# Kernel optimization log

Measured on AMD Instinct MI355X. Metric: run time of the kernel, lower is better.

## Reference

```python
import jax, jax.numpy as jnp
import numpy as np

B, T, D = 2, 1024, 2048
E, K, H = 64, 4, 512          # n_experts, top-k, expert_dim
S, HS = 2, H * K              # shared experts, shared hidden dim
CAP = 512


def setup_inputs() -> dict:
    key = jax.random.key(0)
    ks = jax.random.split(key, 9)
    scale = 0.02
    return {
        "x": jax.random.normal(ks[0], (B, T, D), jnp.float32),
        "Wr": jax.random.normal(ks[1], (D, E), jnp.float32) * scale,
        "router_bias": jnp.zeros((E,), jnp.float32),
        "Wg": jax.random.normal(ks[2], (E, D, H), jnp.float32) * scale,
        "Wu": jax.random.normal(ks[3], (E, D, H), jnp.float32) * scale,
        "Wd": jax.random.normal(ks[4], (E, H, D), jnp.float32) * scale,
        "Sg": jax.random.normal(ks[5], (S, D, HS), jnp.float32) * scale,
        "Su": jax.random.normal(ks[6], (S, D, HS), jnp.float32) * scale,
        "Sd": jax.random.normal(ks[7], (S, HS, D), jnp.float32) * scale,
    }


def reference(x, Wr, router_bias, Wg, Wu, Wd, Sg, Su, Sd):
    Bx, Tx, Dx = x.shape
    N = Bx * Tx
    flat = x.reshape(N, Dx)                              # [N, D]

    # ---- router ----
    logits = flat @ Wr + router_bias                     # [N, E]
    scores = jax.nn.softmax(logits, axis=-1)
    topk_scores, topk_idx = jax.lax.top_k(scores, K)     # [N, K]
    topk_scores = topk_scores / topk_scores.sum(-1, keepdims=True)

    eid = topk_idx.reshape(-1)                           # [N*K] expert per assignment
    w = topk_scores.reshape(-1)                          # [N*K] combine weight
    tok = jnp.repeat(jnp.arange(N), K)                   # [N*K] source token id

    # position of each assignment within its expert's buffer
    oh = jax.nn.one_hot(eid, E, dtype=jnp.int32)         # [N*K, E]
    pos = ((jnp.cumsum(oh, axis=0) * oh).sum(-1) - 1)    # [N*K]
    valid = pos < CAP

    # ---- dispatch: scatter tokens into per-expert buffers ----
    xb = jnp.zeros((E, CAP, Dx), x.dtype).at[eid, pos].set(flat[tok], mode="drop")

    # ---- grouped SwiGLU expert FFN ----
    h = jax.nn.silu(jnp.einsum("ecd,edh->ech", xb, Wg)) * jnp.einsum("ecd,edh->ech", xb, Wu)
    yb = jnp.einsum("ech,ehd->ecd", h, Wd)               # [E, CAP, D]

    # ---- combine: gather back and weighted scatter-add to tokens ----
    y = yb[eid, jnp.minimum(pos, CAP - 1)] * (w * valid)[:, None]
    out = jnp.zeros((N, Dx), x.dtype).at[tok].add(y)

    # ---- always-on shared experts ----
    hs = jax.nn.silu(jnp.einsum("nd,sdh->nsh", flat, Sg)) * jnp.einsum("nd,sdh->nsh", flat, Su)
    out = out + jnp.einsum("nsh,shd->nd", hs, Sd)

    return out.reshape(Bx, Tx, Dx)
```

## Files before the change

### kernel.cpp

```cpp
#include <hip/hip_runtime.h>
#include <hip/hip_bf16.h>
#include <stdint.h>

#define N_TOK 2048
#define DM    2048
#define NEXP  64
#define TOPK  4
#define HEXP  512
#define CAPC  512
#define NSH   2
#define HSH   2048
#define RTB   8

typedef __attribute__((ext_vector_type(8))) short short8;
typedef __attribute__((ext_vector_type(4))) float f32x4;
typedef __attribute__((ext_vector_type(4))) float f4;

#define GLDS16(g, l) __builtin_amdgcn_global_load_lds(                     \
    (const __attribute__((address_space(1))) void*)(g),                    \
    (__attribute__((address_space(3))) void*)(l), 16, 0, 0)

static __device__ __forceinline__ unsigned short f2bf(float f) {
  union { float f; unsigned u; } v; v.f = f;
  unsigned r = v.u + 0x7FFFu + ((v.u >> 16) & 1u);
  return (unsigned short)(r >> 16);
}

__global__ __launch_bounds__(256) void k_convert(const float* __restrict__ x,
                                                 unsigned short* __restrict__ xb) {
  int i = (blockIdx.x * 256 + threadIdx.x) * 8;
  f4 a = *(const f4*)(x + i);
  f4 b = *(const f4*)(x + i + 4);
  short8 o;
  o[0]=f2bf(a[0]); o[1]=f2bf(a[1]); o[2]=f2bf(a[2]); o[3]=f2bf(a[3]);
  o[4]=f2bf(b[0]); o[5]=f2bf(b[1]); o[6]=f2bf(b[2]); o[7]=f2bf(b[3]);
  *(short8*)(xb + i) = o;
}

#define ARGMAX_ROUND(S,I)                                            \
  { float bv = v; int bi = lane;                                     \
    _Pragma("unroll")                                                \
    for (int o = 32; o; o >>= 1) {                                   \
      float ov = __shfl_xor(bv, o); int oi = __shfl_xor(bi, o);      \
      if (ov > bv || (ov == bv && oi < bi)) { bv = ov; bi = oi; }    \
    }                                                                \
    S = bv; I = bi; if (lane == bi) v = -1.f; }

__global__ __launch_bounds__(256) void k_router(const float* __restrict__ x,
    const float* __restrict__ Wr, const float* __restrict__ bias,
    int* __restrict__ cnt, int* __restrict__ lists, float* __restrict__ wlist) {
  __shared__ float part[4][RTB][64];
  __shared__ float logits[RTB][64];
  int t = threadIdx.x;
  int e = t & 63, sl = t >> 6;
  int tok0 = blockIdx.x * RTB;
  const float* xp = x + (size_t)tok0 * DM;
  float acc[RTB];
#pragma unroll
  for (int i = 0; i < RTB; ++i) acc[i] = 0.f;
  for (int d = sl * 512; d < sl * 512 + 512; ++d) {
    float w = Wr[(size_t)d * NEXP + e];
#pragma unroll
    for (int i = 0; i < RTB; ++i) acc[i] += xp[(size_t)i * DM + d] * w;
  }
#pragma unroll
  for (int i = 0; i < RTB; ++i) part[sl][i][e] = acc[i];
  __syncthreads();
  for (int i = sl; i < RTB; i += 4)
    logits[i][e] = part[0][i][e] + part[1][i][e] + part[2][i][e] + part[3][i][e] + bias[e];
  __syncthreads();
  int lane = t & 63, wv = t >> 6;
  for (int i = wv * 2; i < wv * 2 + 2; ++i) {
    float lg = logits[i][lane];
    float m = lg;
#pragma unroll
    for (int o = 32; o; o >>= 1) m = fmaxf(m, __shfl_xor(m, o));
    float p = expf(lg - m);
    float sm = p;
#pragma unroll
    for (int o = 32; o; o >>= 1) sm += __shfl_xor(sm, o);
    float v = p / sm;
    float s0, s1, s2, s3; int i0, i1, i2, i3;
    ARGMAX_ROUND(s0, i0)
    ARGMAX_ROUND(s1, i1)
    ARGMAX_ROUND(s2, i2)
    ARGMAX_ROUND(s3, i3)
    float tot = s0 + s1 + s2 + s3;
    if (lane < TOPK) {
      float myw = (lane == 0 ? s0 : lane == 1 ? s1 : lane == 2 ? s2 : s3) / tot;
      int   mye = (lane == 0 ? i0 : lane == 1 ? i1 : lane == 2 ? i2 : i3);
      int pos = atomicAdd(&cnt[mye], 1);
      if (pos < CAPC) {
        lists[mye * CAPC + pos] = tok0 + i;
        wlist[mye * CAPC + pos] = myw;
      }
    }
  }
}

__global__ void k_offs(const int* __restrict__ cnt, int* __restrict__ offs) {
  int l = threadIdx.x;
  int c = min(cnt[l], CAPC);
  int sum = c;
#pragma unroll
  for (int o = 1; o < 64; o <<= 1) {
    int ov = __shfl_up(sum, o);
    if (l >= o) sum += ov;
  }
  offs[l + 1] = sum;
  if (l == 0) offs[0] = 0;
}


static __device__ __forceinline__ short8 frag_ldA(const unsigned short* lds, int row, int kElem) {
  int byte = row * 128 + kElem * 2;
  byte ^= (row & 7) << 4;
  return *(const short8*)((const char*)lds + byte);
}

static __device__ __forceinline__ short8 bfragB(const float* lB, int nl, int kb) {
  short8 r;
#pragma unroll
  for (int j = 0; j < 8; ++j) r[j] = (short)f2bf(lB[(kb + j) * 64 + nl]);
  return r;
}

static __device__ __forceinline__ void mma1f(const unsigned short* lA, const float* lB,
    f32x4 (&acc)[4][2], int wm, int wn, int lane) {
  int r16 = lane & 15;
  int kg  = (lane >> 4) * 8;
#pragma unroll
  for (int kk = 0; kk < 2; ++kk) {
    int kb = kk * 32 + kg;
    short8 a[4], b[2];
#pragma unroll
    for (int mf = 0; mf < 4; ++mf) a[mf] = frag_ldA(lA, wm + mf * 16 + r16, kb);
#pragma unroll
    for (int nf = 0; nf < 2; ++nf) b[nf] = bfragB(lB, wn + nf * 16 + r16, kb);
#pragma unroll
    for (int mf = 0; mf < 4; ++mf)
#pragma unroll
      for (int nf = 0; nf < 2; ++nf)
        acc[mf][nf] = __builtin_amdgcn_mfma_f32_16x16x32_bf16(a[mf], b[nf], acc[mf][nf], 0, 0, 0);
  }
}

static __device__ __forceinline__ void mma2f(const unsigned short* lA,
    const float* lBg, const float* lBu,
    f32x4 (&accg)[4][2], f32x4 (&accu)[4][2], int wm, int wn, int lane) {
  int r16 = lane & 15;
  int kg  = (lane >> 4) * 8;
#pragma unroll
  for (int kk = 0; kk < 2; ++kk) {
    int kb = kk * 32 + kg;
    short8 a[4], bg[2], bu[2];
#pragma unroll
    for (int mf = 0; mf < 4; ++mf) a[mf] = frag_ldA(lA, wm + mf * 16 + r16, kb);
#pragma unroll
    for (int nf = 0; nf < 2; ++nf) {
      bg[nf] = bfragB(lBg, wn + nf * 16 + r16, kb);
      bu[nf] = bfragB(lBu, wn + nf * 16 + r16, kb);
    }
#pragma unroll
    for (int mf = 0; mf < 4; ++mf)
#pragma unroll
      for (int nf = 0; nf < 2; ++nf) {
        accg[mf][nf] = __builtin_amdgcn_mfma_f32_16x16x32_bf16(a[mf], bg[nf], accg[mf][nf], 0, 0, 0);
        accu[mf][nf] = __builtin_amdgcn_mfma_f32_16x16x32_bf16(a[mf], bu[nf], accu[mf][nf], 0, 0, 0);
      }
  }
}

static __device__ __forceinline__ float silu_mul(float g, float u) {
  return g / (1.f + expf(-g)) * u;
}

#define A_SETUP(asrc, SROW_EXPR)                                            \
  const unsigned short* asrc[4];                                            \
  {                                                                         \
    _Pragma("unroll")                                                       \
    for (int p = 0; p < 4; ++p) {                                           \
      int row = wv * 32 + p * 8 + (lane >> 3);                              \
      int srow = (SROW_EXPR);                                               \
      asrc[p] = Abase + (size_t)srow * lda + (((lane & 7) ^ (row & 7)) << 3);\
    }                                                                       \
  }

#define B_SETUP(bsrc, Bbase, ldb)                                           \
  const float* bsrc[4];                                                     \
  {                                                                         \
    _Pragma("unroll")                                                       \
    for (int p = 0; p < 4; ++p) {                                           \
      int k = wv * 16 + p * 4 + (lane >> 4);                                \
      bsrc[p] = (Bbase) + (size_t)k * (ldb) + n0 + (lane & 15) * 4;         \
    }                                                                       \
  }

#define A_STAGE(asrc, lA, k0)                                               \
  _Pragma("unroll")                                                         \
  for (int p = 0; p < 4; ++p) GLDS16(asrc[p] + (k0), (lA) + wv * 2048 + p * 512);

#define B_STAGE(bsrc, lB, k0, ldb)                                          \
  _Pragma("unroll")                                                         \
  for (int p = 0; p < 4; ++p) GLDS16(bsrc[p] + (size_t)(k0) * (ldb), (lB) + wv * 1024 + p * 256);

__global__ __launch_bounds__(256, 3) void k_expert_gateup(const unsigned short* __restrict__ xbf,
    const float* __restrict__ Wg, const float* __restrict__ Wu,
    const int* __restrict__ cnt, const int* __restrict__ offs,
    const int* __restrict__ lists, unsigned short* __restrict__ hws) {
  int e = blockIdx.y;
  int ne = min(cnt[e], CAPC);
  if (ne == 0) return;
  int n0 = blockIdx.x * 64;
  const float* Bg = Wg + (size_t)e * DM * HEXP;
  const float* Bu = Wu + (size_t)e * DM * HEXP;
  const int* lst = lists + e * CAPC;
  int base = offs[e];
  __shared__ unsigned short lA[128 * 64];
  __shared__ float lBg[64 * 64];
  __shared__ float lBu[64 * 64];
  int tid = threadIdx.x;
  int lane = tid & 63, wv = tid >> 6;
  int wm = (wv >> 1) * 64, wn = (wv & 1) * 32;
  const unsigned short* Abase = xbf; const int lda = DM;
  B_SETUP(bgsrc, Bg, HEXP)
  B_SETUP(busrc, Bu, HEXP)
  for (int m0 = 0; m0 < ne; m0 += 128) {
    A_SETUP(asrc, lst[min(m0 + row, ne - 1)])
    f32x4 accg[4][2] = {};
    f32x4 accu[4][2] = {};
    for (int k0 = 0; k0 < DM; k0 += 64) {
      A_STAGE(asrc, lA, k0)
      B_STAGE(bgsrc, lBg, k0, HEXP)
      B_STAGE(busrc, lBu, k0, HEXP)
      __syncthreads();
      mma2f(lA, lBg, lBu, accg, accu, wm, wn, lane);
      __syncthreads();
    }
#pragma unroll
    for (int mf = 0; mf < 4; ++mf)
#pragma unroll
      for (int r = 0; r < 4; ++r) {
        int rl = m0 + wm + mf * 16 + (lane >> 4) * 4 + r;
        if (rl < ne) {
#pragma unroll
          for (int nf = 0; nf < 2; ++nf) {
            int col = n0 + wn + nf * 16 + (lane & 15);
            float h = silu_mul(accg[mf][nf][r], accu[mf][nf][r]);
            hws[(size_t)(base + rl) * HEXP + col] = f2bf(h);
          }
        }
      }
  }
}

__global__ __launch_bounds__(256, 3) void k_shared_gateup(const unsigned short* __restrict__ xbf,
    const float* __restrict__ Sg, const float* __restrict__ Su,
    unsigned short* __restrict__ hs) {
  int n0 = blockIdx.x * 64;
  int m0 = blockIdx.y * 128;
  int s  = blockIdx.z;
  const float* Bg = Sg + (size_t)s * DM * HSH;
  const float* Bu = Su + (size_t)s * DM * HSH;
  __shared__ unsigned short lA[128 * 64];
  __shared__ float lBg[64 * 64];
  __shared__ float lBu[64 * 64];
  int tid = threadIdx.x;
  int lane = tid & 63, wv = tid >> 6;
  int wm = (wv >> 1) * 64, wn = (wv & 1) * 32;
  const unsigned short* Abase = xbf; const int lda = DM;
  B_SETUP(bgsrc, Bg, HSH)
  B_SETUP(busrc, Bu, HSH)
  A_SETUP(asrc, m0 + row)
  f32x4 accg[4][2] = {};
  f32x4 accu[4][2] = {};
  for (int k0 = 0; k0 < DM; k0 += 64) {
    A_STAGE(asrc, lA, k0)
    B_STAGE(bgsrc, lBg, k0, HSH)
    B_STAGE(busrc, lBu, k0, HSH)
    __syncthreads();
    mma2f(lA, lBg, lBu, accg, accu, wm, wn, lane);
    __syncthreads();
  }
#pragma unroll
  for (int mf = 0; mf < 4; ++mf)
#pragma unroll
    for (int nf = 0; nf < 2; ++nf)
#pragma unroll
      for (int r = 0; r < 4; ++r) {
        int row = m0 + wm + mf * 16 + (lane >> 4) * 4 + r;
        int col = n0 + wn + nf * 16 + (lane & 15);
        float h = silu_mul(accg[mf][nf][r], accu[mf][nf][r]);
        hs[(size_t)row * (NSH * HSH) + s * HSH + col] = f2bf(h);
      }
}

__global__ __launch_bounds__(256, 3) void k_shared_down(const unsigned short* __restrict__ hs,
    const float* __restrict__ Sd, float* __restrict__ out) {
  int n0 = blockIdx.x * 64;
  int m0 = blockIdx.y * 128;
  __shared__ unsigned short lA[128 * 64];
  __shared__ float lB[64 * 64];
  int tid = threadIdx.x;
  int lane = tid & 63, wv = tid >> 6;
  int wm = (wv >> 1) * 64, wn = (wv & 1) * 32;
  const unsigned short* Abase = hs; const int lda = NSH * HSH;
  B_SETUP(bsrc, Sd, DM)
  A_SETUP(asrc, m0 + row)
  f32x4 acc[4][2] = {};
  for (int k0 = 0; k0 < NSH * HSH; k0 += 64) {
    A_STAGE(asrc, lA, k0)
    B_STAGE(bsrc, lB, k0, DM)
    __syncthreads();
    mma1f(lA, lB, acc, wm, wn, lane);
    __syncthreads();
  }
#pragma unroll
  for (int mf = 0; mf < 4; ++mf)
#pragma unroll
    for (int nf = 0; nf < 2; ++nf)
#pragma unroll
      for (int r = 0; r < 4; ++r) {
        int row = m0 + wm + mf * 16 + (lane >> 4) * 4 + r;
        int col = n0 + wn + nf * 16 + (lane & 15);
        out[(size_t)row * DM + col] = acc[mf][nf][r];
      }
}

__global__ __launch_bounds__(256, 3) void k_expert_down(const unsigned short* __restrict__ hws,
    const float* __restrict__ Wd, const int* __restrict__ cnt, const int* __restrict__ offs,
    const int* __restrict__ lists, const float* __restrict__ wlist,
    float* __restrict__ out) {
  int e = blockIdx.y;
  int ne = min(cnt[e], CAPC);
  if (ne == 0) return;
  int n0 = blockIdx.x * 64;
  const float* B = Wd + (size_t)e * HEXP * DM;
  __shared__ unsigned short lA[128 * 64];
  __shared__ float lB[64 * 64];
  int tid = threadIdx.x;
  int lane = tid & 63, wv = tid >> 6;
  int wm = (wv >> 1) * 64, wn = (wv & 1) * 32;
  const unsigned short* Abase = hws + (size_t)offs[e] * HEXP; const int lda = HEXP;
  B_SETUP(bsrc, B, DM)
  for (int m0 = 0; m0 < ne; m0 += 128) {
    A_SETUP(asrc, min(m0 + row, ne - 1))
    f32x4 acc[4][2] = {};
    for (int k0 = 0; k0 < HEXP; k0 += 64) {
      A_STAGE(asrc, lA, k0)
      B_STAGE(bsrc, lB, k0, DM)
      __syncthreads();
      mma1f(lA, lB, acc, wm, wn, lane);
      __syncthreads();
    }
#pragma unroll
    for (int mf = 0; mf < 4; ++mf)
#pragma unroll
      for (int r = 0; r < 4; ++r) {
        int rl = m0 + wm + mf * 16 + (lane >> 4) * 4 + r;
        if (rl < ne) {
          int tok  = lists[e * CAPC + rl];
          float w  = wlist[e * CAPC + rl];
#pragma unroll
          for (int nf = 0; nf < 2; ++nf) {
            int col = n0 + wn + nf * 16 + (lane & 15);
            atomicAdd(out + (size_t)tok * DM + col, acc[mf][nf][r] * w);
          }
        }
      }
  }
}

extern "C" void kernel_launch(void* const* d_in, const int* in_sizes, int n_in,
                              void* d_out, int out_size, void* d_ws, size_t ws_size,
                              hipStream_t stream) {
  const float* x    = (const float*)d_in[0];
  const float* Wr   = (const float*)d_in[1];
  const float* bias = (const float*)d_in[2];
  const float* Wg   = (const float*)d_in[3];
  const float* Wu   = (const float*)d_in[4];
  const float* Wd   = (const float*)d_in[5];
  const float* Sg   = (const float*)d_in[6];
  const float* Su   = (const float*)d_in[7];
  const float* Sd   = (const float*)d_in[8];
  float* out = (float*)d_out;
  char* ws = (char*)d_ws;

  const size_t off_cnt   = 0;
  const size_t off_offs  = 256;
  const size_t off_lists = 1024;
  const size_t off_wlist = off_lists + (size_t)NEXP * CAPC * 4;
  const size_t off_xbf   = off_wlist + (size_t)NEXP * CAPC * 4;
  const size_t off_hs    = off_xbf + (size_t)N_TOK * DM * 2;
  const size_t off_h     = off_hs + (size_t)N_TOK * NSH * HSH * 2;
  const size_t req       = off_h + (size_t)N_TOK * TOPK * HEXP * 2;
  if (ws_size < req) return;

  int* cnt            = (int*)(ws + off_cnt);
  int* offs           = (int*)(ws + off_offs);
  int* lists          = (int*)(ws + off_lists);
  float* wlist        = (float*)(ws + off_wlist);
  unsigned short* xbf = (unsigned short*)(ws + off_xbf);
  unsigned short* hs  = (unsigned short*)(ws + off_hs);
  unsigned short* hws = (unsigned short*)(ws + off_h);

  hipMemsetAsync(cnt, 0, NEXP * sizeof(int), stream);
  k_convert<<<(N_TOK * DM) / (256 * 8), 256, 0, stream>>>(x, xbf);
  k_router<<<N_TOK / RTB, 256, 0, stream>>>(x, Wr, bias, cnt, lists, wlist);
  k_offs<<<1, 64, 0, stream>>>(cnt, offs);
  k_expert_gateup<<<dim3(HEXP / 64, NEXP), 256, 0, stream>>>(xbf, Wg, Wu, cnt, offs, lists, hws);
  k_shared_gateup<<<dim3(HSH / 64, N_TOK / 128, NSH), 256, 0, stream>>>(xbf, Sg, Su, hs);
  k_shared_down<<<dim3(DM / 64, N_TOK / 128), 256, 0, stream>>>(hs, Sd, out);
  k_expert_down<<<dim3(DM / 64, NEXP), 256, 0, stream>>>(hws, Wd, cnt, offs, lists, wlist, out);
}
```

Baseline: 670.9 us.

## Double-buffer LDS staging with BK=32 and swizzled B layout in GEMM kernels

Splits the K-tile from 64 to 32 and double-buffers A/B tiles in LDS so global-to-LDS loads for the next tile overlap MFMA work on the current one, with explicit vmcnt waits and raw barriers in place of __syncthreads. The A and B LDS layouts get new XOR swizzles meant to cut bank conflicts, and B fragment conversion switches to packed v_cvt_pk_bf16_f32. Down-projection kernels raise their occupancy hint to 4 blocks. In exchange there are more barriers per K step and hand-written waitcnt logic, which could race if the counts are wrong.

```diff
diff --git a/kernel.cpp b/kernel.cpp
--- a/kernel.cpp
+++ b/kernel.cpp
@@ -15,10 +15,16 @@
 typedef __attribute__((ext_vector_type(8))) short short8;
 typedef __attribute__((ext_vector_type(4))) float f32x4;
 typedef __attribute__((ext_vector_type(4))) float f4;
+typedef __attribute__((ext_vector_type(4))) unsigned uint4v;
 
 #define GLDS16(g, l) __builtin_amdgcn_global_load_lds(                     \
     (const __attribute__((address_space(1))) void*)(g),                    \
     (__attribute__((address_space(3))) void*)(l), 16, 0, 0)
+
+#define VMWAIT(N) asm volatile("s_waitcnt vmcnt(" #N ")" ::: "memory")
+#define BARX() do { asm volatile("" ::: "memory");                          \
+                    __builtin_amdgcn_s_barrier();                           \
+                    asm volatile("" ::: "memory"); } while (0)
 
 static __device__ __forceinline__ unsigned short f2bf(float f) {
   union { float f; unsigned u; } v; v.f = f;
@@ -113,62 +119,60 @@
 
 
 static __device__ __forceinline__ short8 frag_ldA(const unsigned short* lds, int row, int kElem) {
-  int byte = row * 128 + kElem * 2;
-  byte ^= (row & 7) << 4;
+  int byte = row * 64 + kElem * 2;
+  byte ^= ((row >> 1) & 3) << 4;
   return *(const short8*)((const char*)lds + byte);
 }
 
 static __device__ __forceinline__ short8 bfragB(const float* lB, int nl, int kb) {
-  short8 r;
-#pragma unroll
-  for (int j = 0; j < 8; ++j) r[j] = (short)f2bf(lB[(kb + j) * 64 + nl]);
-  return r;
+  const float* p = lB + kb * 64 + (nl ^ (((kb >> 3) & 1) << 4));
+  float f0 = p[0],   f1 = p[64],  f2 = p[128], f3 = p[192];
+  float f4_ = p[256], f5 = p[320], f6 = p[384], f7 = p[448];
+  unsigned u0, u1, u2, u3;
+  asm("v_cvt_pk_bf16_f32 %0, %1, %2" : "=v"(u0) : "v"(f0),  "v"(f1));
+  asm("v_cvt_pk_bf16_f32 %0, %1, %2" : "=v"(u1) : "v"(f2),  "v"(f3));
+  asm("v_cvt_pk_bf16_f32 %0, %1, %2" : "=v"(u2) : "v"(f4_), "v"(f5));
+  asm("v_cvt_pk_bf16_f32 %0, %1, %2" : "=v"(u3) : "v"(f6),  "v"(f7));
+  uint4v uv = {u0, u1, u2, u3};
+  return __builtin_bit_cast(short8, uv);
 }
 
 static __device__ __forceinline__ void mma1f(const unsigned short* lA, const float* lB,
     f32x4 (&acc)[4][2], int wm, int wn, int lane) {
   int r16 = lane & 15;
-  int kg  = (lane >> 4) * 8;
-#pragma unroll
-  for (int kk = 0; kk < 2; ++kk) {
-    int kb = kk * 32 + kg;
-    short8 a[4], b[2];
-#pragma unroll
-    for (int mf = 0; mf < 4; ++mf) a[mf] = frag_ldA(lA, wm + mf * 16 + r16, kb);
-#pragma unroll
-    for (int nf = 0; nf < 2; ++nf) b[nf] = bfragB(lB, wn + nf * 16 + r16, kb);
-#pragma unroll
-    for (int mf = 0; mf < 4; ++mf)
-#pragma unroll
-      for (int nf = 0; nf < 2; ++nf)
-        acc[mf][nf] = __builtin_amdgcn_mfma_f32_16x16x32_bf16(a[mf], b[nf], acc[mf][nf], 0, 0, 0);
-  }
+  int kb  = (lane >> 4) * 8;
+  short8 a[4], b[2];
+#pragma unroll
+  for (int mf = 0; mf < 4; ++mf) a[mf] = frag_ldA(lA, wm + mf * 16 + r16, kb);
+#pragma unroll
+  for (int nf = 0; nf < 2; ++nf) b[nf] = bfragB(lB, wn + nf * 16 + r16, kb);
+#pragma unroll
+  for (int mf = 0; mf < 4; ++mf)
+#pragma unroll
+    for (int nf = 0; nf < 2; ++nf)
+      acc[mf][nf] = __builtin_amdgcn_mfma_f32_16x16x32_bf16(a[mf], b[nf], acc[mf][nf], 0, 0, 0);
 }
 
 static __device__ __forceinline__ void mma2f(const unsigned short* lA,
     const float* lBg, const float* lBu,
     f32x4 (&accg)[4][2], f32x4 (&accu)[4][2], int wm, int wn, int lane) {
   int r16 = lane & 15;
-  int kg  = (lane >> 4) * 8;
-#pragma unroll
-  for (int kk = 0; kk < 2; ++kk) {
-    int kb = kk * 32 + kg;
-    short8 a[4], bg[2], bu[2];
-#pragma unroll
-    for (int mf = 0; mf < 4; ++mf) a[mf] = frag_ldA(lA, wm + mf * 16 + r16, kb);
+  int kb  = (lane >> 4) * 8;
+  short8 a[4], bg[2], bu[2];
+#pragma unroll
+  for (int mf = 0; mf < 4; ++mf) a[mf] = frag_ldA(lA, wm + mf * 16 + r16, kb);
+#pragma unroll
+  for (int nf = 0; nf < 2; ++nf) {
+    bg[nf] = bfragB(lBg, wn + nf * 16 + r16, kb);
+    bu[nf] = bfragB(lBu, wn + nf * 16 + r16, kb);
+  }
+#pragma unroll
+  for (int mf = 0; mf < 4; ++mf)
 #pragma unroll
     for (int nf = 0; nf < 2; ++nf) {
-      bg[nf] = bfragB(lBg, wn + nf * 16 + r16, kb);
-      bu[nf] = bfragB(lBu, wn + nf * 16 + r16, kb);
-    }
-#pragma unroll
-    for (int mf = 0; mf < 4; ++mf)
-#pragma unroll
-      for (int nf = 0; nf < 2; ++nf) {
-        accg[mf][nf] = __builtin_amdgcn_mfma_f32_16x16x32_bf16(a[mf], bg[nf], accg[mf][nf], 0, 0, 0);
-        accu[mf][nf] = __builtin_amdgcn_mfma_f32_16x16x32_bf16(a[mf], bu[nf], accu[mf][nf], 0, 0, 0);
-      }
-  }
+      accg[mf][nf] = __builtin_amdgcn_mfma_f32_16x16x32_bf16(a[mf], bg[nf], accg[mf][nf], 0, 0, 0);
+      accu[mf][nf] = __builtin_amdgcn_mfma_f32_16x16x32_bf16(a[mf], bu[nf], accu[mf][nf], 0, 0, 0);
+    }
 }
 
 static __device__ __forceinline__ float silu_mul(float g, float u) {
@@ -176,33 +180,35 @@
 }
 
 #define A_SETUP(asrc, SROW_EXPR)                                            \
-  const unsigned short* asrc[4];                                            \
+  const unsigned short* asrc[2];                                            \
   {                                                                         \
     _Pragma("unroll")                                                       \
-    for (int p = 0; p < 4; ++p) {                                           \
-      int row = wv * 32 + p * 8 + (lane >> 3);                              \
+    for (int p = 0; p < 2; ++p) {                                           \
+      int row = p * 64 + wv * 16 + (lane >> 2);                             \
       int srow = (SROW_EXPR);                                               \
-      asrc[p] = Abase + (size_t)srow * lda + (((lane & 7) ^ (row & 7)) << 3);\
+      asrc[p] = Abase + (size_t)srow * lda                                  \
+              + (((lane & 3) ^ ((row >> 1) & 3)) << 3);                     \
     }                                                                       \
   }
+#define A_STAGE(asrc, lAbuf, k0)                                            \
+  { _Pragma("unroll")                                                       \
+    for (int p = 0; p < 2; ++p)                                             \
+      GLDS16(asrc[p] + (k0), (lAbuf) + p * 2048 + wv * 512); }
 
 #define B_SETUP(bsrc, Bbase, ldb)                                           \
-  const float* bsrc[4];                                                     \
+  const float* bsrc[2];                                                     \
   {                                                                         \
     _Pragma("unroll")                                                       \
-    for (int p = 0; p < 4; ++p) {                                           \
-      int k = wv * 16 + p * 4 + (lane >> 4);                                \
-      bsrc[p] = (Bbase) + (size_t)k * (ldb) + n0 + (lane & 15) * 4;         \
+    for (int p = 0; p < 2; ++p) {                                           \
+      int k = p * 16 + wv * 4 + (lane >> 4);                                \
+      int c = (lane & 15) ^ (((k >> 3) & 1) << 2);                          \
+      bsrc[p] = (Bbase) + (size_t)k * (ldb) + n0 + c * 4;                   \
     }                                                                       \
   }
-
-#define A_STAGE(asrc, lA, k0)                                               \
-  _Pragma("unroll")                                                         \
-  for (int p = 0; p < 4; ++p) GLDS16(asrc[p] + (k0), (lA) + wv * 2048 + p * 512);
-
-#define B_STAGE(bsrc, lB, k0, ldb)                                          \
-  _Pragma("unroll")                                                         \
-  for (int p = 0; p < 4; ++p) GLDS16(bsrc[p] + (size_t)(k0) * (ldb), (lB) + wv * 1024 + p * 256);
+#define B_STAGE(bsrc, lBbuf, k0, ldb)                                       \
+  { _Pragma("unroll")                                                       \
+    for (int p = 0; p < 2; ++p)                                             \
+      GLDS16(bsrc[p] + (size_t)(k0) * (ldb), (lBbuf) + p * 1024 + wv * 256); }
 
 __global__ __launch_bounds__(256, 3) void k_expert_gateup(const unsigned short* __restrict__ xbf,
     const float* __restrict__ Wg, const float* __restrict__ Wu,
@@ -216,27 +222,45 @@
   const float* Bu = Wu + (size_t)e * DM * HEXP;
   const int* lst = lists + e * CAPC;
   int base = offs[e];
-  __shared__ unsigned short lA[128 * 64];
-  __shared__ float lBg[64 * 64];
-  __shared__ float lBu[64 * 64];
+  __shared__ unsigned short lA[2][128 * 32];
+  __shared__ float lBg[2][32 * 64];
+  __shared__ float lBu[2][32 * 64];
   int tid = threadIdx.x;
   int lane = tid & 63, wv = tid >> 6;
   int wm = (wv >> 1) * 64, wn = (wv & 1) * 32;
   const unsigned short* Abase = xbf; const int lda = DM;
   B_SETUP(bgsrc, Bg, HEXP)
   B_SETUP(busrc, Bu, HEXP)
+  const int NT = DM / 32;
   for (int m0 = 0; m0 < ne; m0 += 128) {
     A_SETUP(asrc, lst[min(m0 + row, ne - 1)])
     f32x4 accg[4][2] = {};
     f32x4 accu[4][2] = {};
-    for (int k0 = 0; k0 < DM; k0 += 64) {
-      A_STAGE(asrc, lA, k0)
-      B_STAGE(bgsrc, lBg, k0, HEXP)
-      B_STAGE(busrc, lBu, k0, HEXP)
-      __syncthreads();
-      mma2f(lA, lBg, lBu, accg, accu, wm, wn, lane);
-      __syncthreads();
-    }
+    A_STAGE(asrc, lA[0], 0)  B_STAGE(bgsrc, lBg[0], 0, HEXP)  B_STAGE(busrc, lBu[0], 0, HEXP)
+    A_STAGE(asrc, lA[1], 32) B_STAGE(bgsrc, lBg[1], 32, HEXP) B_STAGE(busrc, lBu[1], 32, HEXP)
+    VMWAIT(6); BARX();
+#pragma unroll 1
+    for (int t = 0; t < NT; t += 2) {
+      mma2f(lA[0], lBg[0], lBu[0], accg, accu, wm, wn, lane);
+      BARX();
+      if (t + 2 < NT) {
+        int k2 = (t + 2) * 32;
+        A_STAGE(asrc, lA[0], k2) B_STAGE(bgsrc, lBg[0], k2, HEXP) B_STAGE(busrc, lBu[0], k2, HEXP)
+        VMWAIT(6);
+      } else { VMWAIT(0); }
+      BARX();
+      mma2f(lA[1], lBg[1], lBu[1], accg, accu, wm, wn, lane);
+      if (t + 2 < NT) {
+        BARX();
+        if (t + 3 < NT) {
+          int k3 = (t + 3) * 32;
+          A_STAGE(asrc, lA[1], k3) B_STAGE(bgsrc, lBg[1], k3, HEXP) B_STAGE(busrc, lBu[1], k3, HEXP)
+          VMWAIT(6);
+        } else { VMWAIT(0); }
+        BARX();
+      }
+    }
+    BARX();
 #pragma unroll
     for (int mf = 0; mf < 4; ++mf)
 #pragma unroll
@@ -262,9 +286,9 @@
   int s  = blockIdx.z;
   const float* Bg = Sg + (size_t)s * DM * HSH;
   const float* Bu = Su + (size_t)s * DM * HSH;
-  __shared__ unsigned short lA[128 * 64];
-  __shared__ float lBg[64 * 64];
-  __shared__ float lBu[64 * 64];
+  __shared__ unsigned short lA[2][128 * 32];
+  __shared__ float lBg[2][32 * 64];
+  __shared__ float lBu[2][32 * 64];
   int tid = threadIdx.x;
   int lane = tid & 63, wv = tid >> 6;
   int wm = (wv >> 1) * 64, wn = (wv & 1) * 32;
@@ -274,13 +298,30 @@
   A_SETUP(asrc, m0 + row)
   f32x4 accg[4][2] = {};
   f32x4 accu[4][2] = {};
-  for (int k0 = 0; k0 < DM; k0 += 64) {
-    A_STAGE(asrc, lA, k0)
-    B_STAGE(bgsrc, lBg, k0, HSH)
-    B_STAGE(busrc, lBu, k0, HSH)
-    __syncthreads();
-    mma2f(lA, lBg, lBu, accg, accu, wm, wn, lane);
-    __syncthreads();
+  const int NT = DM / 32;
+  A_STAGE(asrc, lA[0], 0)  B_STAGE(bgsrc, lBg[0], 0, HSH)  B_STAGE(busrc, lBu[0], 0, HSH)
+  A_STAGE(asrc, lA[1], 32) B_STAGE(bgsrc, lBg[1], 32, HSH) B_STAGE(busrc, lBu[1], 32, HSH)
+  VMWAIT(6); BARX();
+#pragma unroll 1
+  for (int t = 0; t < NT; t += 2) {
+    mma2f(lA[0], lBg[0], lBu[0], accg, accu, wm, wn, lane);
+    BARX();
+    if (t + 2 < NT) {
+      int k2 = (t + 2) * 32;
+      A_STAGE(asrc, lA[0], k2) B_STAGE(bgsrc, lBg[0], k2, HSH) B_STAGE(busrc, lBu[0], k2, HSH)
+      VMWAIT(6);
+    } else { VMWAIT(0); }
+    BARX();
+    mma2f(lA[1], lBg[1], lBu[1], accg, accu, wm, wn, lane);
+    if (t + 2 < NT) {
+      BARX();
+      if (t + 3 < NT) {
+        int k3 = (t + 3) * 32;
+        A_STAGE(asrc, lA[1], k3) B_STAGE(bgsrc, lBg[1], k3, HSH) B_STAGE(busrc, lBu[1], k3, HSH)
+        VMWAIT(6);
+      } else { VMWAIT(0); }
+      BARX();
+    }
   }
 #pragma unroll
   for (int mf = 0; mf < 4; ++mf)
@@ -295,12 +336,12 @@
       }
 }
 
-__global__ __launch_bounds__(256, 3) void k_shared_down(const unsigned short* __restrict__ hs,
+__global__ __launch_bounds__(256, 4) void k_shared_down(const unsigned short* __restrict__ hs,
     const float* __restrict__ Sd, float* __restrict__ out) {
   int n0 = blockIdx.x * 64;
   int m0 = blockIdx.y * 128;
-  __shared__ unsigned short lA[128 * 64];
-  __shared__ float lB[64 * 64];
+  __shared__ unsigned short lA[2][128 * 32];
+  __shared__ float lB[2][32 * 64];
   int tid = threadIdx.x;
   int lane = tid & 63, wv = tid >> 6;
   int wm = (wv >> 1) * 64, wn = (wv & 1) * 32;
@@ -308,12 +349,30 @@
   B_SETUP(bsrc, Sd, DM)
   A_SETUP(asrc, m0 + row)
   f32x4 acc[4][2] = {};
-  for (int k0 = 0; k0 < NSH * HSH; k0 += 64) {
-    A_STAGE(asrc, lA, k0)
-    B_STAGE(bsrc, lB, k0, DM)
-    __syncthreads();
-    mma1f(lA, lB, acc, wm, wn, lane);
-    __syncthreads();
+  const int NT = (NSH * HSH) / 32;
+  A_STAGE(asrc, lA[0], 0)  B_STAGE(bsrc, lB[0], 0, DM)
+  A_STAGE(asrc, lA[1], 32) B_STAGE(bsrc, lB[1], 32, DM)
+  VMWAIT(4); BARX();
+#pragma unroll 1
+  for (int t = 0; t < NT; t += 2) {
+    mma1f(lA[0], lB[0], acc, wm, wn, lane);
+    BARX();
+    if (t + 2 < NT) {
+      int k2 = (t + 2) * 32;
+      A_STAGE(asrc, lA[0], k2) B_STAGE(bsrc, lB[0], k2, DM)
+      VMWAIT(4);
+    } else { VMWAIT(0); }
+    BARX();
+    mma1f(lA[1], lB[1], acc, wm, wn, lane);
+    if (t + 2 < NT) {
+      BARX();
+      if (t + 3 < NT) {
+        int k3 = (t + 3) * 32;
+        A_STAGE(asrc, lA[1], k3) B_STAGE(bsrc, lB[1], k3, DM)
+        VMWAIT(4);
+      } else { VMWAIT(0); }
+      BARX();
+    }
   }
 #pragma unroll
   for (int mf = 0; mf < 4; ++mf)
@@ -327,7 +386,7 @@
       }
 }
 
-__global__ __launch_bounds__(256, 3) void k_expert_down(const unsigned short* __restrict__ hws,
+__global__ __launch_bounds__(256, 4) void k_expert_down(const unsigned short* __restrict__ hws,
     const float* __restrict__ Wd, const int* __restrict__ cnt, const int* __restrict__ offs,
     const int* __restrict__ lists, const float* __restrict__ wlist,
     float* __restrict__ out) {
@@ -336,23 +395,42 @@
   if (ne == 0) return;
   int n0 = blockIdx.x * 64;
   const float* B = Wd + (size_t)e * HEXP * DM;
-  __shared__ unsigned short lA[128 * 64];
-  __shared__ float lB[64 * 64];
+  __shared__ unsigned short lA[2][128 * 32];
+  __shared__ float lB[2][32 * 64];
   int tid = threadIdx.x;
   int lane = tid & 63, wv = tid >> 6;
   int wm = (wv >> 1) * 64, wn = (wv & 1) * 32;
   const unsigned short* Abase = hws + (size_t)offs[e] * HEXP; const int lda = HEXP;
   B_SETUP(bsrc, B, DM)
+  const int NT = HEXP / 32;
   for (int m0 = 0; m0 < ne; m0 += 128) {
     A_SETUP(asrc, min(m0 + row, ne - 1))
     f32x4 acc[4][2] = {};
-    for (int k0 = 0; k0 < HEXP; k0 += 64) {
-      A_STAGE(asrc, lA, k0)
-      B_STAGE(bsrc, lB, k0, DM)
-      __syncthreads();
-      mma1f(lA, lB, acc, wm, wn, lane);
-      __syncthreads();
-    }
+    A_STAGE(asrc, lA[0], 0)  B_STAGE(bsrc, lB[0], 0, DM)
+    A_STAGE(asrc, lA[1], 32) B_STAGE(bsrc, lB[1], 32, DM)
+    VMWAIT(4); BARX();
+#pragma unroll 1
+    for (int t = 0; t < NT; t += 2) {
+      mma1f(lA[0], lB[0], acc, wm, wn, lane);
+      BARX();
+      if (t + 2 < NT) {
+        int k2 = (t + 2) * 32;
+        A_STAGE(asrc, lA[0], k2) B_STAGE(bsrc, lB[0], k2, DM)
+        VMWAIT(4);
+      } else { VMWAIT(0); }
+      BARX();
+      mma1f(lA[1], lB[1], acc, wm, wn, lane);
+      if (t + 2 < NT) {
+        BARX();
+        if (t + 3 < NT) {
+          int k3 = (t + 3) * 32;
+          A_STAGE(asrc, lA[1], k3) B_STAGE(bsrc, lB[1], k3, DM)
+          VMWAIT(4);
+        } else { VMWAIT(0); }
+        BARX();
+      }
+    }
+    BARX();
 #pragma unroll
     for (int mf = 0; mf < 4; ++mf)
 #pragma unroll
```

Result: no change. 662.5 us (-1.2%).
